# Kernel tuning notes

Measured on AMD Instinct MI355X. Metric: run time of the kernel, lower is better.

The kernel has to match this reference:

```python
import jax, jax.numpy as jnp
import numpy as np

D_MODEL = 1024
N_HEADS = 16
D_FF = 4096
B = 8
S_TGT = 1024
S_SRC = 1024


def layer_norm(x, g, b, eps=1e-5):
    mu = jnp.mean(x, axis=-1, keepdims=True)
    var = jnp.mean(jnp.square(x - mu), axis=-1, keepdims=True)
    return (x - mu) * jax.lax.rsqrt(var + eps) * g + b


def mha(q_in, k_in, v_in, Wq, bq, Wk, bk, Wv, bv, Wo, bo, mask):
    Bq, Sq, D = q_in.shape
    hd = D // N_HEADS

    def split(t):
        return t.reshape(t.shape[0], t.shape[1], N_HEADS, hd).transpose(0, 2, 1, 3)

    Q = split(q_in @ Wq + bq)   # [B,H,Sq,hd]
    K = split(k_in @ Wk + bk)   # [B,H,Sk,hd]
    V = split(v_in @ Wv + bv)
    scores = jnp.einsum('bhqd,bhkd->bhqk', Q, K) / jnp.sqrt(jnp.float32(hd))
    scores = jnp.where(mask, scores, jnp.float32(-1e9))
    attn = jax.nn.softmax(scores, axis=-1)
    out = jnp.einsum('bhqk,bhkd->bhqd', attn, V)
    out = out.transpose(0, 2, 1, 3).reshape(Bq, Sq, D)
    return out @ Wo + bo


def setup_inputs() -> dict:
    key = jax.random.key(0)
    ks = jax.random.split(key, 32)
    s = 0.02
    inp = {
        'x': jax.random.normal(ks[0], (B, S_TGT, D_MODEL), dtype=jnp.float32),
        'encoder_output': jax.random.normal(ks[1], (B, S_SRC, D_MODEL), dtype=jnp.float32),
        'tgt_mask': jnp.tril(jnp.ones((S_TGT, S_TGT), dtype=bool))[None, None],
        'src_mask': jnp.ones((1, 1, S_TGT, S_SRC), dtype=bool),
    }
    i = 2
    for p in ('sa', 'ca'):
        for w in ('Wq', 'Wk', 'Wv', 'Wo'):
            inp[f'{p}_{w}'] = jax.random.normal(ks[i], (D_MODEL, D_MODEL), dtype=jnp.float32) * s
            inp[f'{p}_b{w[1].lower()}'] = jnp.zeros((D_MODEL,), dtype=jnp.float32)
            i += 1
    inp['ff_W1'] = jax.random.normal(ks[i], (D_MODEL, D_FF), dtype=jnp.float32) * s; i += 1
    inp['ff_b1'] = jnp.zeros((D_FF,), dtype=jnp.float32)
    inp['ff_W2'] = jax.random.normal(ks[i], (D_FF, D_MODEL), dtype=jnp.float32) * s; i += 1
    inp['ff_b2'] = jnp.zeros((D_MODEL,), dtype=jnp.float32)
    for n in ('ln1', 'ln2', 'ln3'):
        inp[f'{n}_g'] = jnp.ones((D_MODEL,), dtype=jnp.float32)
        inp[f'{n}_b'] = jnp.zeros((D_MODEL,), dtype=jnp.float32)
    return inp


def reference(x, encoder_output, tgt_mask, src_mask,
              sa_Wq, sa_bq, sa_Wk, sa_bk, sa_Wv, sa_bv, sa_Wo, sa_bo,
              ca_Wq, ca_bq, ca_Wk, ca_bk, ca_Wv, ca_bv, ca_Wo, ca_bo,
              ff_W1, ff_b1, ff_W2, ff_b2,
              ln1_g, ln1_b, ln2_g, ln2_b, ln3_g, ln3_b):
    # masked self-attention + residual + LN (dropout = identity in eval mode)
    attn = mha(x, x, x, sa_Wq, sa_bq, sa_Wk, sa_bk, sa_Wv, sa_bv, sa_Wo, sa_bo, tgt_mask)
    x = layer_norm(x + attn, ln1_g, ln1_b)
    # cross-attention to encoder output
    cross = mha(x, encoder_output, encoder_output,
                ca_Wq, ca_bq, ca_Wk, ca_bk, ca_Wv, ca_bv, ca_Wo, ca_bo, src_mask)
    x = layer_norm(x + cross, ln2_g, ln2_b)
    # position-wise FFN: Linear -> ReLU -> Linear
    ff = jax.nn.relu(x @ ff_W1 + ff_b1) @ ff_W2 + ff_b2
    x = layer_norm(x + ff, ln3_g, ln3_b)
    return x
```

## Files before the change

kernel.cpp:

```cpp
#include <hip/hip_runtime.h>
#include <math.h>

typedef __attribute__((ext_vector_type(8))) short short8;
typedef __attribute__((ext_vector_type(4))) short short4v;
typedef __attribute__((ext_vector_type(4))) float floatx4;

__device__ inline float bf2f(unsigned short h) {
    unsigned int u = ((unsigned int)h) << 16;
    float f;
    __builtin_memcpy(&f, &u, 4);
    return f;
}
__device__ inline unsigned short f2bf(float f) {
    unsigned int u;
    __builtin_memcpy(&u, &f, 4);
    u = (u + 0x7fffu + ((u >> 16) & 1u)) >> 16;
    return (unsigned short)u;
}
__device__ inline unsigned int f2u(float f) {
    return __builtin_bit_cast(unsigned int, f);
}

__device__ inline void gld_lds16(const unsigned short* g, unsigned short* l) {
    __builtin_amdgcn_global_load_lds(
        (const __attribute__((address_space(1))) unsigned int*)g,
        (__attribute__((address_space(3))) unsigned int*)l, 16, 0, 0);
}

__global__ __launch_bounds__(256) void detect_dtype(
    const unsigned short* __restrict__ x, int* __restrict__ flag) {
    __shared__ int s[4];
    int bad = 0;
    for (int i = threadIdx.x; i < 8192; i += 256) {
        float v = bf2f(x[i]);
        if (!(fabsf(v) <= 1.0e4f)) bad = 1;
    }
    unsigned long long b = __ballot(bad);
    int wave = threadIdx.x >> 6;
    if ((threadIdx.x & 63) == 0) s[wave] = (b != 0ULL) ? 1 : 0;
    __syncthreads();
    if (threadIdx.x == 0) flag[0] = s[0] | s[1] | s[2] | s[3];
}

__global__ __launch_bounds__(256) void to_bf16_kernel(
    const void* __restrict__ in, unsigned short* __restrict__ out,
    const int* __restrict__ flag, int n8) {
    int fl = flag[0];
    int i = blockIdx.x * 256 + threadIdx.x;
    if (i >= n8) return;
    size_t off = (size_t)i * 8;
    if (fl) {
        floatx4 f0 = *(const floatx4*)((const float*)in + off);
        floatx4 f1 = *(const floatx4*)((const float*)in + off + 4);
        short8 v;
#pragma unroll
        for (int j = 0; j < 4; j++) {
            v[j] = (short)f2bf(f0[j]);
            v[4 + j] = (short)f2bf(f1[j]);
        }
        *(short8*)(out + off) = v;
    } else {
        *(short8*)(out + off) = *(const short8*)((const unsigned short*)in + off);
    }
}

__global__ __launch_bounds__(256) void transpose_any(
    const void* __restrict__ in, unsigned short* __restrict__ out,
    int rows, int cols, const int* __restrict__ flag) {
    int fl = flag ? flag[0] : 0;
    __shared__ unsigned short t[32][33];
    int tx = threadIdx.x & 31, ty = threadIdx.x >> 5;
    int c0 = blockIdx.x * 32, r0 = blockIdx.y * 32;
    size_t base = (size_t)blockIdx.z * rows * cols;
#pragma unroll
    for (int k = 0; k < 4; k++) {
        size_t idx = base + (size_t)(r0 + ty + k * 8) * cols + c0 + tx;
        t[ty + k * 8][tx] = fl ? f2bf(((const float*)in)[idx])
                               : ((const unsigned short*)in)[idx];
    }
    __syncthreads();
#pragma unroll
    for (int k = 0; k < 4; k++)
        out[base + (size_t)(c0 + ty + k * 8) * rows + r0 + tx] = t[tx][ty + k * 8];
}

__device__ inline void stage_half(const unsigned short* __restrict__ G, int ldk,
                                  int grow, int gcol, unsigned short* ldsb,
                                  int tid) {
    int s0 = tid, s1 = tid + 512;
    int r0 = s0 >> 3, c0 = ((s0 & 7) ^ (r0 & 7)) << 3;
    int r1 = s1 >> 3, c1 = ((s1 & 7) ^ (r1 & 7)) << 3;
    gld_lds16(&G[(size_t)(grow + r0) * ldk + gcol + c0], &ldsb[s0 * 8]);
    gld_lds16(&G[(size_t)(grow + r1) * ldk + gcol + c1], &ldsb[s1 * 8]);
}

template <int BN_, int EPI>
__global__ __launch_bounds__(512) void gemm8(
    const unsigned short* __restrict__ A, const unsigned short* __restrict__ Bt,
    const void* __restrict__ b0, const void* __restrict__ b1,
    const void* __restrict__ b2, unsigned short* __restrict__ C0,
    unsigned short* __restrict__ C1, unsigned short* __restrict__ C2,
    int M, int N, int K, const int* __restrict__ flag) {
    constexpr int NR = BN_ / 64;
    constexpr int WNT = BN_ / 4;
    constexpr int ASZ = 16384;
    constexpr int BSZ = BN_ * 64;
    __shared__ alignas(16) unsigned short lds[2 * ASZ + 2 * BSZ];

    const int tid = threadIdx.x;
    const int lane = tid & 63, wave = tid >> 6;
    const int quad = lane >> 4, l16 = lane & 15, x7 = l16 & 7;
    const int wm = wave >> 2, wn = wave & 3;
    const int bm = blockIdx.x * 256, bn = blockIdx.y * BN_;
    const int NT = K >> 6;

    floatx4 acc[8][NR];
#pragma unroll
    for (int i = 0; i < 8; ++i)
#pragma unroll
        for (int j = 0; j < NR; ++j) acc[i][j] = (floatx4){0.f, 0.f, 0.f, 0.f};

    stage_half(A, K, bm, 0, lds, tid);
    stage_half(A, K, bm + 128, 0, lds + 8192, tid);
    stage_half(Bt, K, bn, 0, lds + 2 * ASZ, tid);
    if (BN_ == 256) stage_half(Bt, K, bn + 128, 0, lds + 2 * ASZ + 8192, tid);
    asm volatile("s_waitcnt vmcnt(0)" ::: "memory");
    __builtin_amdgcn_s_barrier();

    short8 bfr[NR][2], afr[2][2][2];

    for (int it = 0; it < NT; ++it) {
        unsigned short* const Ac = lds + (it & 1) * ASZ;
        unsigned short* const Bc = lds + 2 * ASZ + (it & 1) * BSZ;
        unsigned short* const An = lds + ((it + 1) & 1) * ASZ;
        unsigned short* const Bn = lds + 2 * ASZ + ((it + 1) & 1) * BSZ;
        const bool more = (it + 1 < NT);
        if (more) {
            const int kn = (it + 1) << 6;
            stage_half(A, K, bm, kn, An, tid);
            stage_half(A, K, bm + 128, kn, An + 8192, tid);
            stage_half(Bt, K, bn, kn, Bn, tid);
            if (BN_ == 256) stage_half(Bt, K, bn + 128, kn, Bn + 8192, tid);
        }
#pragma unroll
        for (int ni = 0; ni < NR; ++ni)
#pragma unroll
            for (int ks = 0; ks < 2; ++ks)
                bfr[ni][ks] = *(const short8*)&Bc[
                    (wn * WNT + ni * 16 + l16) * 64 +
                    ((((ks << 2) + quad) ^ x7) << 3)];
#pragma unroll
        for (int m2 = 0; m2 < 2; ++m2)
#pragma unroll
            for (int ks = 0; ks < 2; ++ks)
                afr[0][m2][ks] = *(const short8*)&Ac[
                    (wm * 128 + m2 * 16 + l16) * 64 +
                    ((((ks << 2) + quad) ^ x7) << 3)];
#pragma unroll
        for (int q = 0; q < 4; ++q) {
            if (q < 3) {
#pragma unroll
                for (int m2 = 0; m2 < 2; ++m2)
#pragma unroll
                    for (int ks = 0; ks < 2; ++ks)
                        afr[(q + 1) & 1][m2][ks] = *(const short8*)&Ac[
                            (wm * 128 + ((q + 1) * 2 + m2) * 16 + l16) * 64 +
                            ((((ks << 2) + quad) ^ x7) << 3)];
            }
            __builtin_amdgcn_s_setprio(1);
#pragma unroll
            for (int m2 = 0; m2 < 2; ++m2)
#pragma unroll
                for (int ni = 0; ni < NR; ++ni) {
                    acc[q * 2 + m2][ni] = __builtin_amdgcn_mfma_f32_16x16x32_bf16(
                        bfr[ni][0], afr[q & 1][m2][0], acc[q * 2 + m2][ni], 0, 0, 0);
                    acc[q * 2 + m2][ni] = __builtin_amdgcn_mfma_f32_16x16x32_bf16(
                        bfr[ni][1], afr[q & 1][m2][1], acc[q * 2 + m2][ni], 0, 0, 0);
                }
            __builtin_amdgcn_s_setprio(0);
        }
        if (more) {
            asm volatile("s_waitcnt vmcnt(0)" ::: "memory");
            __builtin_amdgcn_s_barrier();
        }
    }

    const int fl = flag[0];
    const void* bp = b0;
    unsigned short* Cp = C0;
    int mode = 0;
    int cb = bn;
    if (EPI == 1) mode = 1;
    if (EPI == 4) mode = 2;
    if (EPI == 2) {
        int ch = bn >> 10;
        cb = bn & 1023;
        bp = (ch == 0) ? b0 : (ch == 1) ? b1 : b2;
        Cp = (ch == 0) ? C0 : (ch == 1) ? C1 : C2;
        mode = (ch == 0) ? 2 : (ch == 1) ? 3 : 4;
    }
    if (EPI == 3) {
        int ch = bn >> 10;
        cb = bn & 1023;
        bp = (ch == 0) ? b0 : b1;
        Cp = (ch == 0) ? C0 : C1;
        mode = (ch == 0) ? 3 : 4;
    }
#pragma unroll
    for (int ni = 0; ni < NR; ++ni) {
        const int colb = cb + wn * WNT + ni * 16 + quad * 4;
        float b4[4];
        if (fl) {
            floatx4 t = *(const floatx4*)&((const float*)bp)[colb];
#pragma unroll
            for (int r = 0; r < 4; ++r) b4[r] = t[r];
        } else {
            short4v t = *(const short4v*)&((const unsigned short*)bp)[colb];
#pragma unroll
            for (int r = 0; r < 4; ++r) b4[r] = bf2f((unsigned short)t[r]);
        }
        const int hh = colb >> 6, dd = colb & 63;
#pragma unroll
        for (int mi = 0; mi < 8; ++mi) {
            const int row = bm + wm * 128 + mi * 16 + l16;
            short4v pk;
#pragma unroll
            for (int r = 0; r < 4; ++r) {
                float v = acc[mi][ni][r] + b4[r];
                if (mode == 1) v = fmaxf(v, 0.f);
                if (mode == 2) v *= 0.18033688f;
                pk[r] = (short)f2bf(v);
            }
            if (mode <= 1) {
                *(short4v*)&Cp[(size_t)row * N + colb] = pk;
            } else {
                const int b_ = row >> 10, s_ = row & 1023;
                if (mode != 4) {
                    *(short4v*)&Cp[((((size_t)b_ * 16 + hh) * 1024) + s_) * 64 + dd] = pk;
                } else {
#pragma unroll
                    for (int r = 0; r < 4; ++r)
                        Cp[(((size_t)b_ * 16 + hh) * 64 + dd + r) * 1024 + s_] =
                            (unsigned short)pk[r];
                }
            }
        }
    }
}

template <int CAUSAL>
__global__ __launch_bounds__(256) void attn_kernel(
    const unsigned short* __restrict__ Q, const unsigned short* __restrict__ K,
    const unsigned short* __restrict__ Vt, unsigned short* __restrict__ O,
    int Skv) {
    __shared__ alignas(16) unsigned short Ks[512 * 8];
    __shared__ alignas(16) unsigned short Vs[512 * 8];
    const int S = 1024;
    int tid = threadIdx.x, wave = tid >> 6, lane = tid & 63;
    int quad = lane >> 4, l16 = lane & 15;
    int bh = blockIdx.y, bx = blockIdx.x;
    int qbase = bx * 64 + wave * 16;
    const unsigned short* Qp = Q + (size_t)bh * S * 64;
    const unsigned short* Kp = K + (size_t)bh * Skv * 64;
    const unsigned short* Vp = Vt + (size_t)bh * 64 * Skv;

    short8 qf0 = *(const short8*)&Qp[(qbase + l16) * 64 + quad * 8];
    short8 qf1 = *(const short8*)&Qp[(qbase + l16) * 64 + 32 + quad * 8];

    floatx4 o[4];
#pragma unroll
    for (int ni = 0; ni < 4; ni++) o[ni] = (floatx4){0.f, 0.f, 0.f, 0.f};
    float m = -1e30f, l = 0.f;
    int kend = CAUSAL ? (bx + 1) * 64 : Skv;

    int sr0 = tid >> 3, sc0 = (tid & 7) ^ (sr0 & 7);
    int sr1 = (tid + 256) >> 3, sc1 = ((tid + 256) & 7) ^ (sr1 & 7);
    int shA = l16 + (((2 * quad) & 3) << 4);
    int shB = l16 + (((2 * quad + 1) & 3) << 4);

    for (int kb = 0; kb < kend; kb += 64) {
        gld_lds16(&Kp[(size_t)(kb + sr0) * 64 + sc0 * 8], &Ks[tid * 8]);
        gld_lds16(&Kp[(size_t)(kb + sr1) * 64 + sc1 * 8], &Ks[(tid + 256) * 8]);
        gld_lds16(&Vp[(size_t)sr0 * Skv + kb + sc0 * 8], &Vs[tid * 8]);
        gld_lds16(&Vp[(size_t)sr1 * Skv + kb + sc1 * 8], &Vs[(tid + 256) * 8]);
        __syncthreads();

        floatx4 st[4];
#pragma unroll
        for (int c = 0; c < 4; c++) {
            int row = c * 16 + l16, r7 = row & 7;
            short8 kf0 = *(const short8*)&Ks[(row * 8 + (quad ^ r7)) * 8];
            short8 kf1 = *(const short8*)&Ks[(row * 8 + ((quad + 4) ^ r7)) * 8];
            floatx4 z = (floatx4){0.f, 0.f, 0.f, 0.f};
            z = __builtin_amdgcn_mfma_f32_16x16x32_bf16(kf0, qf0, z, 0, 0, 0);
            z = __builtin_amdgcn_mfma_f32_16x16x32_bf16(kf1, qf1, z, 0, 0, 0);
            st[c] = z;
        }
        if (CAUSAL && (kb + 63 > qbase)) {
#pragma unroll
            for (int c = 0; c < 4; c++)
#pragma unroll
                for (int r = 0; r < 4; r++) {
                    int kk = kb + c * 16 + quad * 4 + r;
                    if (kk > qbase + l16) st[c][r] = -1e30f;
                }
        }
        floatx4 t01, t23;
#pragma unroll
        for (int r = 0; r < 4; r++) {
            t01[r] = fmaxf(st[0][r], st[1][r]);
            t23[r] = fmaxf(st[2][r], st[3][r]);
        }
        float smax = fmaxf(fmaxf(fmaxf(t01[0], t01[1]), fmaxf(t01[2], t01[3])),
                           fmaxf(fmaxf(t23[0], t23[1]), fmaxf(t23[2], t23[3])));
        smax = fmaxf(smax, __shfl_xor(smax, 16));
        smax = fmaxf(smax, __shfl_xor(smax, 32));
        float mi = fmaxf(m, smax);
        float alpha = exp2f(m - mi);
        float rs = 0.f;
#pragma unroll
        for (int c = 0; c < 4; c++)
#pragma unroll
            for (int r = 0; r < 4; r++) {
                float p = exp2f(st[c][r] - mi);
                st[c][r] = p;
                rs += p;
            }
        rs += __shfl_xor(rs, 16);
        rs += __shfl_xor(rs, 32);
        l = l * alpha + rs;
        m = mi;
#pragma unroll
        for (int ni = 0; ni < 4; ni++) o[ni] *= alpha;

        unsigned int pd[4][2];
#pragma unroll
        for (int c = 0; c < 4; c++) {
            float e0 = st[c][0], e1 = st[c][1], e2 = st[c][2], e3 = st[c][3];
            pd[c][0] = __builtin_amdgcn_perm(f2u(e1), f2u(e0), 0x07060302u);
            pd[c][1] = __builtin_amdgcn_perm(f2u(e3), f2u(e2), 0x07060302u);
        }
        short8 pf[2];
#pragma unroll
        for (int h = 0; h < 2; h++) {
            unsigned int a0 = __shfl((int)pd[2 * h][0], shA);
            unsigned int a1 = __shfl((int)pd[2 * h][1], shA);
            unsigned int a2 = __shfl((int)pd[2 * h][0], shB);
            unsigned int a3 = __shfl((int)pd[2 * h][1], shB);
            unsigned int b0 = __shfl((int)pd[2 * h + 1][0], shA);
            unsigned int b1 = __shfl((int)pd[2 * h + 1][1], shA);
            unsigned int b2 = __shfl((int)pd[2 * h + 1][0], shB);
            unsigned int b3 = __shfl((int)pd[2 * h + 1][1], shB);
            unsigned int dw[4];
            dw[0] = (quad < 2) ? a0 : b0;
            dw[1] = (quad < 2) ? a1 : b1;
            dw[2] = (quad < 2) ? a2 : b2;
            dw[3] = (quad < 2) ? a3 : b3;
            __builtin_memcpy(&pf[h], dw, 16);
        }
#pragma unroll
        for (int ni = 0; ni < 4; ni++) {
            int row = ni * 16 + l16, r7 = row & 7;
            short8 vf0 = *(const short8*)&Vs[(row * 8 + (quad ^ r7)) * 8];
            short8 vf1 = *(const short8*)&Vs[(row * 8 + ((quad + 4) ^ r7)) * 8];
            o[ni] = __builtin_amdgcn_mfma_f32_16x16x32_bf16(vf0, pf[0], o[ni], 0, 0, 0);
            o[ni] = __builtin_amdgcn_mfma_f32_16x16x32_bf16(vf1, pf[1], o[ni], 0, 0, 0);
        }
        __syncthreads();
    }

    int b = bh >> 4, h = bh & 15;
    float inv = 1.0f / l;
    size_t qrow = ((size_t)(b * S + qbase + l16)) * 1024 + h * 64;
#pragma unroll
    for (int ni = 0; ni < 4; ni++) {
        short4v p4;
#pragma unroll
        for (int r = 0; r < 4; r++) p4[r] = (short)f2bf(o[ni][r] * inv);
        *(short4v*)&O[qrow + ni * 16 + quad * 4] = p4;
    }
}

template <int AEXT, int OEXT>
__global__ __launch_bounds__(256) void add_ln_kernel(
    const void* __restrict__ A, const unsigned short* __restrict__ Bv,
    const void* __restrict__ g, const void* __restrict__ be,
    void* __restrict__ out, const int* __restrict__ flag) {
    int fl = flag[0];
    __shared__ float red[2][4];
    int row = blockIdx.x, tid = threadIdx.x;
    size_t base = (size_t)row * 1024;
    int c = tid * 4;
    float v[4], sum = 0.f, ss = 0.f;
    if (AEXT && fl) {
        floatx4 af = *(const floatx4*)&((const float*)A)[base + c];
#pragma unroll
        for (int k = 0; k < 4; k++) v[k] = af[k];
    } else {
        short4v av = *(const short4v*)&((const unsigned short*)A)[base + c];
#pragma unroll
        for (int k = 0; k < 4; k++) v[k] = bf2f((unsigned short)av[k]);
    }
    short4v bv = *(const short4v*)&Bv[base + c];
#pragma unroll
    for (int k = 0; k < 4; k++) {
        v[k] += bf2f((unsigned short)bv[k]);
        sum += v[k];
        ss += v[k] * v[k];
    }
#pragma unroll
    for (int off = 1; off < 64; off <<= 1) {
        sum += __shfl_xor(sum, off);
        ss += __shfl_xor(ss, off);
    }
    int wave = tid >> 6, lane = tid & 63;
    if (lane == 0) {
        red[0][wave] = sum;
        red[1][wave] = ss;
    }
    __syncthreads();
    sum = red[0][0] + red[0][1] + red[0][2] + red[0][3];
    ss = red[1][0] + red[1][1] + red[1][2] + red[1][3];
    float mu = sum * (1.0f / 1024.0f);
    float var = ss * (1.0f / 1024.0f) - mu * mu;
    float rstd = rsqrtf(var + 1e-5f);
#pragma unroll
    for (int k = 0; k < 4; k++) {
        float gv = fl ? ((const float*)g)[c + k]
                      : bf2f(((const unsigned short*)g)[c + k]);
        float bev = fl ? ((const float*)be)[c + k]
                       : bf2f(((const unsigned short*)be)[c + k]);
        float y = (v[k] - mu) * rstd * gv + bev;
        if (OEXT && fl)
            ((float*)out)[base + c + k] = y;
        else
            ((unsigned short*)out)[base + c + k] = f2bf(y);
    }
}

extern "C" void kernel_launch(void* const* d_in, const int* in_sizes, int n_in,
                              void* d_out, int out_size, void* d_ws, size_t ws_size,
                              hipStream_t stream) {
    const int M = 8192;
    typedef const void* cvp;
    cvp x = d_in[0];
    cvp enc = d_in[1];
    cvp saWq = d_in[4], sabq = d_in[5];
    cvp saWk = d_in[6], sabk = d_in[7];
    cvp saWv = d_in[8], sabv = d_in[9];
    cvp saWo = d_in[10], sabo = d_in[11];
    cvp caWq = d_in[12], cabq = d_in[13];
    cvp caWk = d_in[14], cabk = d_in[15];
    cvp caWv = d_in[16], cabv = d_in[17];
    cvp caWo = d_in[18], cabo = d_in[19];
    cvp ffW1 = d_in[20], ffb1 = d_in[21];
    cvp ffW2 = d_in[22], ffb2 = d_in[23];
    cvp ln1g = d_in[24], ln1b = d_in[25];
    cvp ln2g = d_in[26], ln2b = d_in[27];
    cvp ln3g = d_in[28], ln3b = d_in[29];

    char* ws = (char*)d_ws;
    const size_t MB = 1024 * 1024;
    typedef unsigned short* up;
    up wt_sa_qkv = (up)(ws + 0);
    up wt_sa_o   = (up)(ws + 6 * MB);
    up wt_ca_q   = (up)(ws + 8 * MB);
    up wt_ca_kv  = (up)(ws + 10 * MB);
    up wt_ca_o   = (up)(ws + 14 * MB);
    up wtff1     = (up)(ws + 16 * MB);
    up wtff2     = (up)(ws + 24 * MB);
    up Qb  = (up)(ws + 32 * MB);
    up Kb  = (up)(ws + 48 * MB);
    up Vtb = (up)(ws + 64 * MB);
    up xb  = (up)(ws + 80 * MB);
    up Hb  = (up)(ws + 32 * MB);
    up Ob  = (up)(ws + 96 * MB);
    up Pb  = (up)(ws + 112 * MB);
    up x1  = (up)(ws + 128 * MB);
    up x2  = (up)(ws + 144 * MB);
    up encb = (up)(ws + 144 * MB);
    int* flag = (int*)(ws + 160 * MB);

    dim3 blk(256), blk5(512);
    detect_dtype<<<1, blk, 0, stream>>>((const unsigned short*)x, flag);

    to_bf16_kernel<<<4096, blk, 0, stream>>>(x, xb, flag, M * 1024 / 8);
    to_bf16_kernel<<<4096, blk, 0, stream>>>(enc, encb, flag, M * 1024 / 8);

    transpose_any<<<dim3(32, 32, 1), blk, 0, stream>>>(saWq, wt_sa_qkv, 1024, 1024, flag);
    transpose_any<<<dim3(32, 32, 1), blk, 0, stream>>>(saWk, wt_sa_qkv + 1024 * 1024, 1024, 1024, flag);
    transpose_any<<<dim3(32, 32, 1), blk, 0, stream>>>(saWv, wt_sa_qkv + 2 * 1024 * 1024, 1024, 1024, flag);
    transpose_any<<<dim3(32, 32, 1), blk, 0, stream>>>(saWo, wt_sa_o, 1024, 1024, flag);
    transpose_any<<<dim3(32, 32, 1), blk, 0, stream>>>(caWq, wt_ca_q, 1024, 1024, flag);
    transpose_any<<<dim3(32, 32, 1), blk, 0, stream>>>(caWk, wt_ca_kv, 1024, 1024, flag);
    transpose_any<<<dim3(32, 32, 1), blk, 0, stream>>>(caWv, wt_ca_kv + 1024 * 1024, 1024, 1024, flag);
    transpose_any<<<dim3(32, 32, 1), blk, 0, stream>>>(caWo, wt_ca_o, 1024, 1024, flag);
    transpose_any<<<dim3(128, 32, 1), blk, 0, stream>>>(ffW1, wtff1, 1024, 4096, flag);
    transpose_any<<<dim3(32, 128, 1), blk, 0, stream>>>(ffW2, wtff2, 4096, 1024, flag);

    gemm8<256, 2><<<dim3(32, 12), blk5, 0, stream>>>(
        xb, wt_sa_qkv, sabq, sabk, sabv, Qb, Kb, Vtb, M, 3072, 1024, flag);
    attn_kernel<1><<<dim3(16, 128), blk, 0, stream>>>(Qb, Kb, Vtb, Ob, 1024);
    gemm8<128, 0><<<dim3(32, 8), blk5, 0, stream>>>(
        Ob, wt_sa_o, sabo, nullptr, nullptr, Pb, nullptr, nullptr, M, 1024, 1024, flag);
    add_ln_kernel<1, 0><<<dim3(8192), blk, 0, stream>>>(x, Pb, ln1g, ln1b, x1, flag);

    gemm8<128, 4><<<dim3(32, 8), blk5, 0, stream>>>(
        x1, wt_ca_q, cabq, nullptr, nullptr, Qb, nullptr, nullptr, M, 1024, 1024, flag);
    gemm8<256, 3><<<dim3(32, 8), blk5, 0, stream>>>(
        encb, wt_ca_kv, cabk, cabv, nullptr, Kb, Vtb, nullptr, M, 2048, 1024, flag);
    attn_kernel<0><<<dim3(16, 128), blk, 0, stream>>>(Qb, Kb, Vtb, Ob, 1024);
    gemm8<128, 0><<<dim3(32, 8), blk5, 0, stream>>>(
        Ob, wt_ca_o, cabo, nullptr, nullptr, Pb, nullptr, nullptr, M, 1024, 1024, flag);
    add_ln_kernel<0, 0><<<dim3(8192), blk, 0, stream>>>(x1, Pb, ln2g, ln2b, x2, flag);

    gemm8<256, 1><<<dim3(32, 16), blk5, 0, stream>>>(
        x2, wtff1, ffb1, nullptr, nullptr, Hb, nullptr, nullptr, M, 4096, 1024, flag);
    gemm8<128, 0><<<dim3(32, 8), blk5, 0, stream>>>(
        Hb, wtff2, ffb2, nullptr, nullptr, Pb, nullptr, nullptr, M, 1024, 4096, flag);
    add_ln_kernel<0, 1><<<dim3(8192), blk, 0, stream>>>(x2, Pb, ln3g, ln3b, d_out, flag);
}
```

Before: 820.0 us.

## Process two query tiles per wave in attention and batch weight transposes

The attention kernel now handles 128 query rows per block, two 16-row tiles per wave, so each K/V tile staged in LDS is reused twice. Blocks are reordered so heavy causal tiles launch first, and fully masked sub-tiles are skipped. A lazy softmax rescale only rescales the output when the running max grows by more than a threshold. The eight square weight transposes are merged into one launch. In exchange the kernel uses more registers and runs half as many blocks, and the transpose8 output is hardcoded to workspace offset 0, which assumes the weight buffers sit there contiguously.

New measurement: 774.4 us. -5.6%, faster.

```diff
diff --git a/kernel.cpp b/kernel.cpp
--- a/kernel.cpp
+++ b/kernel.cpp
@@ -82,6 +82,27 @@
 #pragma unroll
     for (int k = 0; k < 4; k++)
         out[base + (size_t)(c0 + ty + k * 8) * rows + r0 + tx] = t[tx][ty + k * 8];
+}
+
+struct Ptr8 { const void* p[8]; };
+__global__ __launch_bounds__(256) void transpose8(
+    Ptr8 in, unsigned short* __restrict__ out, const int* __restrict__ flag) {
+    int fl = flag[0];
+    __shared__ unsigned short t[32][33];
+    const void* src = in.p[blockIdx.z];
+    unsigned short* dst = out + (size_t)blockIdx.z * 1024 * 1024;
+    int tx = threadIdx.x & 31, ty = threadIdx.x >> 5;
+    int c0 = blockIdx.x * 32, r0 = blockIdx.y * 32;
+#pragma unroll
+    for (int k = 0; k < 4; k++) {
+        size_t idx = (size_t)(r0 + ty + k * 8) * 1024 + c0 + tx;
+        t[ty + k * 8][tx] = fl ? f2bf(((const float*)src)[idx])
+                               : ((const unsigned short*)src)[idx];
+    }
+    __syncthreads();
+#pragma unroll
+    for (int k = 0; k < 4; k++)
+        dst[(size_t)(c0 + ty + k * 8) * 1024 + r0 + tx] = t[tx][ty + k * 8];
 }
 
 __device__ inline void stage_half(const unsigned short* __restrict__ G, int ldk,
@@ -258,20 +279,29 @@
     const int S = 1024;
     int tid = threadIdx.x, wave = tid >> 6, lane = tid & 63;
     int quad = lane >> 4, l16 = lane & 15;
-    int bh = blockIdx.y, bx = blockIdx.x;
-    int qbase = bx * 64 + wave * 16;
+    int fid = blockIdx.y * 8 + blockIdx.x;
+    int bh = fid & 127;
+    int qt = fid >> 7;
+    if (CAUSAL) qt = 7 - qt;
+    int qbA = qt * 128 + wave * 32;
+    int qbB = qbA + 16;
     const unsigned short* Qp = Q + (size_t)bh * S * 64;
     const unsigned short* Kp = K + (size_t)bh * Skv * 64;
     const unsigned short* Vp = Vt + (size_t)bh * 64 * Skv;
 
-    short8 qf0 = *(const short8*)&Qp[(qbase + l16) * 64 + quad * 8];
-    short8 qf1 = *(const short8*)&Qp[(qbase + l16) * 64 + 32 + quad * 8];
-
-    floatx4 o[4];
-#pragma unroll
-    for (int ni = 0; ni < 4; ni++) o[ni] = (floatx4){0.f, 0.f, 0.f, 0.f};
-    float m = -1e30f, l = 0.f;
-    int kend = CAUSAL ? (bx + 1) * 64 : Skv;
+    short8 qA0 = *(const short8*)&Qp[(qbA + l16) * 64 + quad * 8];
+    short8 qA1 = *(const short8*)&Qp[(qbA + l16) * 64 + 32 + quad * 8];
+    short8 qB0 = *(const short8*)&Qp[(qbB + l16) * 64 + quad * 8];
+    short8 qB1 = *(const short8*)&Qp[(qbB + l16) * 64 + 32 + quad * 8];
+
+    floatx4 oA[4], oB[4];
+#pragma unroll
+    for (int ni = 0; ni < 4; ni++) {
+        oA[ni] = (floatx4){0.f, 0.f, 0.f, 0.f};
+        oB[ni] = (floatx4){0.f, 0.f, 0.f, 0.f};
+    }
+    float mA = -1e30f, lA = 0.f, mB = -1e30f, lB = 0.f;
+    int kend = CAUSAL ? (qt + 1) * 128 : Skv;
 
     int sr0 = tid >> 3, sc0 = (tid & 7) ^ (sr0 & 7);
     int sr1 = (tid + 256) >> 3, sc1 = ((tid + 256) & 7) ^ (sr1 & 7);
@@ -285,99 +315,113 @@
         gld_lds16(&Vp[(size_t)sr1 * Skv + kb + sc1 * 8], &Vs[(tid + 256) * 8]);
         __syncthreads();
 
-        floatx4 st[4];
-#pragma unroll
-        for (int c = 0; c < 4; c++) {
-            int row = c * 16 + l16, r7 = row & 7;
-            short8 kf0 = *(const short8*)&Ks[(row * 8 + (quad ^ r7)) * 8];
-            short8 kf1 = *(const short8*)&Ks[(row * 8 + ((quad + 4) ^ r7)) * 8];
-            floatx4 z = (floatx4){0.f, 0.f, 0.f, 0.f};
-            z = __builtin_amdgcn_mfma_f32_16x16x32_bf16(kf0, qf0, z, 0, 0, 0);
-            z = __builtin_amdgcn_mfma_f32_16x16x32_bf16(kf1, qf1, z, 0, 0, 0);
-            st[c] = z;
-        }
-        if (CAUSAL && (kb + 63 > qbase)) {
+        auto tile = [&](const short8& q0, const short8& q1, floatx4(&o)[4],
+                        float& m, float& l, int qb) {
+            if (CAUSAL && kb > qb + 15) return;
+            floatx4 st[4];
+#pragma unroll
+            for (int c = 0; c < 4; c++) {
+                int row = c * 16 + l16, r7 = row & 7;
+                short8 kf0 = *(const short8*)&Ks[(row * 8 + (quad ^ r7)) * 8];
+                short8 kf1 = *(const short8*)&Ks[(row * 8 + ((quad + 4) ^ r7)) * 8];
+                floatx4 z = (floatx4){0.f, 0.f, 0.f, 0.f};
+                z = __builtin_amdgcn_mfma_f32_16x16x32_bf16(kf0, q0, z, 0, 0, 0);
+                z = __builtin_amdgcn_mfma_f32_16x16x32_bf16(kf1, q1, z, 0, 0, 0);
+                st[c] = z;
+            }
+            if (CAUSAL && (kb + 63 > qb)) {
+#pragma unroll
+                for (int c = 0; c < 4; c++)
+#pragma unroll
+                    for (int r = 0; r < 4; r++) {
+                        int kk = kb + c * 16 + quad * 4 + r;
+                        if (kk > qb + l16) st[c][r] = -1e30f;
+                    }
+            }
+            float t0 = fmaxf(fmaxf(st[0][0], st[0][1]), st[0][2]);
+            float t1 = fmaxf(fmaxf(st[0][3], st[1][0]), st[1][1]);
+            float t2 = fmaxf(fmaxf(st[1][2], st[1][3]), st[2][0]);
+            float t3 = fmaxf(fmaxf(st[2][1], st[2][2]), st[2][3]);
+            float t4 = fmaxf(fmaxf(st[3][0], st[3][1]), st[3][2]);
+            float smax = fmaxf(fmaxf(fmaxf(t0, t1), fmaxf(t2, t3)),
+                               fmaxf(t4, st[3][3]));
+            smax = fmaxf(smax, __shfl_xor(smax, 16));
+            smax = fmaxf(smax, __shfl_xor(smax, 32));
+            float mi = m;
+            if (!__all(smax <= m + 8.f)) {
+                mi = fmaxf(m, smax);
+                float alpha = exp2f(m - mi);
+                l *= alpha;
+#pragma unroll
+                for (int ni = 0; ni < 4; ni++) o[ni] *= alpha;
+                m = mi;
+            }
+            float rs = 0.f;
 #pragma unroll
             for (int c = 0; c < 4; c++)
 #pragma unroll
                 for (int r = 0; r < 4; r++) {
-                    int kk = kb + c * 16 + quad * 4 + r;
-                    if (kk > qbase + l16) st[c][r] = -1e30f;
+                    float p = exp2f(st[c][r] - mi);
+                    st[c][r] = p;
+                    rs += p;
                 }
-        }
-        floatx4 t01, t23;
-#pragma unroll
-        for (int r = 0; r < 4; r++) {
-            t01[r] = fmaxf(st[0][r], st[1][r]);
-            t23[r] = fmaxf(st[2][r], st[3][r]);
-        }
-        float smax = fmaxf(fmaxf(fmaxf(t01[0], t01[1]), fmaxf(t01[2], t01[3])),
-                           fmaxf(fmaxf(t23[0], t23[1]), fmaxf(t23[2], t23[3])));
-        smax = fmaxf(smax, __shfl_xor(smax, 16));
-        smax = fmaxf(smax, __shfl_xor(smax, 32));
-        float mi = fmaxf(m, smax);
-        float alpha = exp2f(m - mi);
-        float rs = 0.f;
-#pragma unroll
-        for (int c = 0; c < 4; c++)
-#pragma unroll
-            for (int r = 0; r < 4; r++) {
-                float p = exp2f(st[c][r] - mi);
-                st[c][r] = p;
-                rs += p;
-            }
-        rs += __shfl_xor(rs, 16);
-        rs += __shfl_xor(rs, 32);
-        l = l * alpha + rs;
-        m = mi;
-#pragma unroll
-        for (int ni = 0; ni < 4; ni++) o[ni] *= alpha;
-
-        unsigned int pd[4][2];
-#pragma unroll
-        for (int c = 0; c < 4; c++) {
-            float e0 = st[c][0], e1 = st[c][1], e2 = st[c][2], e3 = st[c][3];
-            pd[c][0] = __builtin_amdgcn_perm(f2u(e1), f2u(e0), 0x07060302u);
-            pd[c][1] = __builtin_amdgcn_perm(f2u(e3), f2u(e2), 0x07060302u);
-        }
-        short8 pf[2];
-#pragma unroll
-        for (int h = 0; h < 2; h++) {
-            unsigned int a0 = __shfl((int)pd[2 * h][0], shA);
-            unsigned int a1 = __shfl((int)pd[2 * h][1], shA);
-            unsigned int a2 = __shfl((int)pd[2 * h][0], shB);
-            unsigned int a3 = __shfl((int)pd[2 * h][1], shB);
-            unsigned int b0 = __shfl((int)pd[2 * h + 1][0], shA);
-            unsigned int b1 = __shfl((int)pd[2 * h + 1][1], shA);
-            unsigned int b2 = __shfl((int)pd[2 * h + 1][0], shB);
-            unsigned int b3 = __shfl((int)pd[2 * h + 1][1], shB);
-            unsigned int dw[4];
-            dw[0] = (quad < 2) ? a0 : b0;
-            dw[1] = (quad < 2) ? a1 : b1;
-            dw[2] = (quad < 2) ? a2 : b2;
-            dw[3] = (quad < 2) ? a3 : b3;
-            __builtin_memcpy(&pf[h], dw, 16);
-        }
-#pragma unroll
-        for (int ni = 0; ni < 4; ni++) {
-            int row = ni * 16 + l16, r7 = row & 7;
-            short8 vf0 = *(const short8*)&Vs[(row * 8 + (quad ^ r7)) * 8];
-            short8 vf1 = *(const short8*)&Vs[(row * 8 + ((quad + 4) ^ r7)) * 8];
-            o[ni] = __builtin_amdgcn_mfma_f32_16x16x32_bf16(vf0, pf[0], o[ni], 0, 0, 0);
-            o[ni] = __builtin_amdgcn_mfma_f32_16x16x32_bf16(vf1, pf[1], o[ni], 0, 0, 0);
-        }
+            rs += __shfl_xor(rs, 16);
+            rs += __shfl_xor(rs, 32);
+            l += rs;
+
+            unsigned int pd[4][2];
+#pragma unroll
+            for (int c = 0; c < 4; c++) {
+                pd[c][0] = __builtin_amdgcn_perm(f2u(st[c][1]), f2u(st[c][0]),
+                                                 0x07060302u);
+                pd[c][1] = __builtin_amdgcn_perm(f2u(st[c][3]), f2u(st[c][2]),
+                                                 0x07060302u);
+            }
+            short8 pf[2];
+#pragma unroll
+            for (int h = 0; h < 2; h++) {
+                unsigned int a0 = __shfl((int)pd[2 * h][0], shA);
+                unsigned int a1 = __shfl((int)pd[2 * h][1], shA);
+                unsigned int a2 = __shfl((int)pd[2 * h][0], shB);
+                unsigned int a3 = __shfl((int)pd[2 * h][1], shB);
+                unsigned int b0 = __shfl((int)pd[2 * h + 1][0], shA);
+                unsigned int b1 = __shfl((int)pd[2 * h + 1][1], shA);
+                unsigned int b2 = __shfl((int)pd[2 * h + 1][0], shB);
+                unsigned int b3 = __shfl((int)pd[2 * h + 1][1], shB);
+                unsigned int dw[4];
+                dw[0] = (quad < 2) ? a0 : b0;
+                dw[1] = (quad < 2) ? a1 : b1;
+                dw[2] = (quad < 2) ? a2 : b2;
+                dw[3] = (quad < 2) ? a3 : b3;
+                __builtin_memcpy(&pf[h], dw, 16);
+            }
+#pragma unroll
+            for (int ni = 0; ni < 4; ni++) {
+                int row = ni * 16 + l16, r7 = row & 7;
+                short8 vf0 = *(const short8*)&Vs[(row * 8 + (quad ^ r7)) * 8];
+                short8 vf1 = *(const short8*)&Vs[(row * 8 + ((quad + 4) ^ r7)) * 8];
+                o[ni] = __builtin_amdgcn_mfma_f32_16x16x32_bf16(vf0, pf[0], o[ni], 0, 0, 0);
+                o[ni] = __builtin_amdgcn_mfma_f32_16x16x32_bf16(vf1, pf[1], o[ni], 0, 0, 0);
+            }
+        };
+        tile(qA0, qA1, oA, mA, lA, qbA);
+        tile(qB0, qB1, oB, mB, lB, qbB);
         __syncthreads();
     }
 
     int b = bh >> 4, h = bh & 15;
-    float inv = 1.0f / l;
-    size_t qrow = ((size_t)(b * S + qbase + l16)) * 1024 + h * 64;
+    float invA = 1.0f / lA, invB = 1.0f / lB;
+    size_t qrowA = ((size_t)(b * S + qbA + l16)) * 1024 + h * 64;
+    size_t qrowB = ((size_t)(b * S + qbB + l16)) * 1024 + h * 64;
 #pragma unroll
     for (int ni = 0; ni < 4; ni++) {
         short4v p4;
 #pragma unroll
-        for (int r = 0; r < 4; r++) p4[r] = (short)f2bf(o[ni][r] * inv);
-        *(short4v*)&O[qrow + ni * 16 + quad * 4] = p4;
+        for (int r = 0; r < 4; r++) p4[r] = (short)f2bf(oA[ni][r] * invA);
+        *(short4v*)&O[qrowA + ni * 16 + quad * 4] = p4;
+#pragma unroll
+        for (int r = 0; r < 4; r++) p4[r] = (short)f2bf(oB[ni][r] * invB);
+        *(short4v*)&O[qrowB + ni * 16 + quad * 4] = p4;
     }
 }
 
@@ -487,20 +531,16 @@
     to_bf16_kernel<<<4096, blk, 0, stream>>>(x, xb, flag, M * 1024 / 8);
     to_bf16_kernel<<<4096, blk, 0, stream>>>(enc, encb, flag, M * 1024 / 8);
 
-    transpose_any<<<dim3(32, 32, 1), blk, 0, stream>>>(saWq, wt_sa_qkv, 1024, 1024, flag);
-    transpose_any<<<dim3(32, 32, 1), blk, 0, stream>>>(saWk, wt_sa_qkv + 1024 * 1024, 1024, 1024, flag);
-    transpose_any<<<dim3(32, 32, 1), blk, 0, stream>>>(saWv, wt_sa_qkv + 2 * 1024 * 1024, 1024, 1024, flag);
-    transpose_any<<<dim3(32, 32, 1), blk, 0, stream>>>(saWo, wt_sa_o, 1024, 1024, flag);
-    transpose_any<<<dim3(32, 32, 1), blk, 0, stream>>>(caWq, wt_ca_q, 1024, 1024, flag);
-    transpose_any<<<dim3(32, 32, 1), blk, 0, stream>>>(caWk, wt_ca_kv, 1024, 1024, flag);
-    transpose_any<<<dim3(32, 32, 1), blk, 0, stream>>>(caWv, wt_ca_kv + 1024 * 1024, 1024, 1024, flag);
-    transpose_any<<<dim3(32, 32, 1), blk, 0, stream>>>(caWo, wt_ca_o, 1024, 1024, flag);
+    Ptr8 w8;
+    w8.p[0] = saWq; w8.p[1] = saWk; w8.p[2] = saWv; w8.p[3] = saWo;
+    w8.p[4] = caWq; w8.p[5] = caWk; w8.p[6] = caWv; w8.p[7] = caWo;
+    transpose8<<<dim3(32, 32, 8), blk, 0, stream>>>(w8, (up)(ws + 0), flag);
     transpose_any<<<dim3(128, 32, 1), blk, 0, stream>>>(ffW1, wtff1, 1024, 4096, flag);
     transpose_any<<<dim3(32, 128, 1), blk, 0, stream>>>(ffW2, wtff2, 4096, 1024, flag);
 
     gemm8<256, 2><<<dim3(32, 12), blk5, 0, stream>>>(
         xb, wt_sa_qkv, sabq, sabk, sabv, Qb, Kb, Vtb, M, 3072, 1024, flag);
-    attn_kernel<1><<<dim3(16, 128), blk, 0, stream>>>(Qb, Kb, Vtb, Ob, 1024);
+    attn_kernel<1><<<dim3(8, 128), blk, 0, stream>>>(Qb, Kb, Vtb, Ob, 1024);
     gemm8<128, 0><<<dim3(32, 8), blk5, 0, stream>>>(
         Ob, wt_sa_o, sabo, nullptr, nullptr, Pb, nullptr, nullptr, M, 1024, 1024, flag);
     add_ln_kernel<1, 0><<<dim3(8192), blk, 0, stream>>>(x, Pb, ln1g, ln1b, x1, flag);
@@ -509,7 +549,7 @@
         x1, wt_ca_q, cabq, nullptr, nullptr, Qb, nullptr, nullptr, M, 1024, 1024, flag);
     gemm8<256, 3><<<dim3(32, 8), blk5, 0, stream>>>(
         encb, wt_ca_kv, cabk, cabv, nullptr, Kb, Vtb, nullptr, M, 2048, 1024, flag);
-    attn_kernel<0><<<dim3(16, 128), blk, 0, stream>>>(Qb, Kb, Vtb, Ob, 1024);
+    attn_kernel<0><<<dim3(8, 128), blk, 0, stream>>>(Qb, Kb, Vtb, Ob, 1024);
     gemm8<128, 0><<<dim3(32, 8), blk5, 0, stream>>>(
         Ob, wt_ca_o, cabo, nullptr, nullptr, Pb, nullptr, nullptr, M, 1024, 1024, flag);
     add_ln_kernel<0, 0><<<dim3(8192), blk, 0, stream>>>(x1, Pb, ln2g, ln2b, x2, flag);
```
